# Performance work log

Hardware: AMD Instinct MI355X
Metric: run time of the kernel (lower is better)

The kernel has to match this reference:

```python
import jax, jax.numpy as jnp
import numpy as np

N = 100000
E = 1600000
B = 64
NUM_CLASSES = 10


def setup_inputs() -> dict:
    key = jax.random.key(0)
    ks = jax.random.split(key, 8)
    x = jax.random.normal(ks[0], (N, 5), dtype=jnp.float32)
    edge_index = jax.random.randint(ks[1], (2, E), 0, N, dtype=jnp.int64)
    batch = jnp.sort(jax.random.randint(ks[2], (N,), 0, B, dtype=jnp.int64))

    def glorot(k, fan_in, fan_out):
        s = jnp.sqrt(6.0 / (fan_in + fan_out)).astype(jnp.float32)
        return jax.random.uniform(k, (fan_in, fan_out), jnp.float32, -s, s)

    dims = [(5, 32), (32, 64), (64, 128), (128, 256)]
    Ws = [glorot(jax.random.fold_in(ks[3], i), a, b) for i, (a, b) in enumerate(dims)]
    bs = [jnp.zeros((b,), jnp.float32) for (_, b) in dims]
    fc1_w = glorot(ks[4], 256, 100)
    fc1_b = jnp.zeros((100,), jnp.float32)
    fc2_w = glorot(ks[5], 100, NUM_CLASSES)
    fc2_b = jnp.zeros((NUM_CLASSES,), jnp.float32)
    return {
        'x': x, 'edge_index': edge_index, 'batch': batch,
        'W1': Ws[0], 'b1': bs[0], 'W2': Ws[1], 'b2': bs[1],
        'W3': Ws[2], 'b3': bs[2], 'W4': Ws[3], 'b4': bs[3],
        'fc1_w': fc1_w, 'fc1_b': fc1_b, 'fc2_w': fc2_w, 'fc2_b': fc2_b,
    }


def _gcn_conv(x, W, b, src, dst, dinv):
    h = x @ W                                   # [N, out]
    norm = (dinv[src] * dinv[dst])[:, None]      # [E, 1]
    msg = h[src] * norm                          # gather + scale
    agg = jax.ops.segment_sum(msg, dst, num_segments=N)
    agg = agg + h * (dinv * dinv)[:, None]       # self-loop contribution
    return agg + b


def reference(x, edge_index, batch, W1, b1, W2, b2, W3, b3, W4, b4,
              fc1_w, fc1_b, fc2_w, fc2_b):
    src, dst = edge_index[0], edge_index[1]
    # degree including self-loop
    deg = jax.ops.segment_sum(jnp.ones((E,), jnp.float32), dst, num_segments=N) + 1.0
    dinv = jax.lax.rsqrt(deg)

    h = jax.nn.relu(_gcn_conv(x, W1, b1, src, dst, dinv))
    # mesh_unpool with pool target 0 -> identity
    h = jax.nn.relu(_gcn_conv(h, W2, b2, src, dst, dinv))
    h = jax.nn.relu(_gcn_conv(h, W3, b3, src, dst, dinv))
    h = jax.nn.relu(_gcn_conv(h, W4, b4, src, dst, dinv))

    # global mean pool over graphs
    sums = jax.ops.segment_sum(h, batch, num_segments=B)
    cnt = jax.ops.segment_sum(jnp.ones((N,), jnp.float32), batch, num_segments=B)
    pooled = sums / jnp.maximum(cnt, 1.0)[:, None]

    h = jax.nn.relu(pooled @ fc1_w + fc1_b)
    return jax.nn.log_softmax(h @ fc2_w + fc2_b, axis=-1)
```

## Files before the change

kernel.cpp:

```cpp
#include <hip/hip_runtime.h>
#include <hip/hip_bf16.h>
#include <cmath>

#define NN 100000
#define NE 1600000
#define NBATCH 64
#define NB 391
#define NBP 512
#define BCAP 5120
#define NPAD (NB * BCAP)

typedef __attribute__((ext_vector_type(8))) short bf16x8;
typedef __attribute__((ext_vector_type(4))) float f32x4;

__device__ __forceinline__ void atomAdd(float* p, float v) {
  unsafeAtomicAdd(p, v);
}

__device__ __forceinline__ unsigned short f2bf(float f) {
  __hip_bfloat16 h = __float2bfloat16(f);
  union { __hip_bfloat16 h; unsigned short u; } cv; cv.h = h; return cv.u;
}
__device__ __forceinline__ float bflo(unsigned int u) { return __uint_as_float(u << 16); }
__device__ __forceinline__ float bfhi(unsigned int u) { return __uint_as_float(u & 0xffff0000u); }

__global__ __launch_bounds__(256) void k_bin(const int* __restrict__ src,
    const int* __restrict__ dst, int* __restrict__ bucketCnt, uint2* __restrict__ pairs,
    const float* __restrict__ W2, const float* __restrict__ W3, const float* __restrict__ W4,
    unsigned short* __restrict__ Wt2, unsigned short* __restrict__ Wt3,
    unsigned short* __restrict__ Wt4) {
  __shared__ int hist[NBP];
  __shared__ int scn[NBP];
  __shared__ int ofs[NBP];
  __shared__ int gbase[NBP];
  __shared__ uint2 buf[4096];
  const int base = blockIdx.x * 4096;
  const int n = (NE - base < 4096) ? NE - base : 4096;
  for (int i = threadIdx.x; i < NBP; i += 256) hist[i] = 0;
  __syncthreads();

  int myS[16], myD[16];
  int nloc = 0;
  for (int i = threadIdx.x, j = 0; i < n; i += 256, ++j) {
    myS[j] = src[base + i];
    myD[j] = dst[base + i];
    atomicAdd(&hist[myD[j] >> 8], 1);
    nloc = j + 1;
  }
  __syncthreads();

  scn[threadIdx.x] = hist[threadIdx.x];
  scn[threadIdx.x + 256] = hist[threadIdx.x + 256];
  __syncthreads();
  for (int off = 1; off < NBP; off <<= 1) {
    const int i0 = threadIdx.x, i1 = threadIdx.x + 256;
    int t0 = (i0 >= off) ? scn[i0 - off] : 0;
    int t1 = (i1 >= off) ? scn[i1 - off] : 0;
    __syncthreads();
    scn[i0] += t0;
    scn[i1] += t1;
    __syncthreads();
  }
  ofs[threadIdx.x] = scn[threadIdx.x] - hist[threadIdx.x];
  ofs[threadIdx.x + 256] = scn[threadIdx.x + 256] - hist[threadIdx.x + 256];
  for (int b = threadIdx.x; b < NB; b += 256) {
    int c = hist[b];
    if (c) gbase[b] = b * BCAP + atomicAdd(&bucketCnt[b], c);
  }
  __syncthreads();

  for (int j = 0; j < nloc; ++j) {
    int b = myD[j] >> 8;
    int slot = atomicAdd(&ofs[b], 1);
    buf[slot] = make_uint2((unsigned)myS[j], (unsigned)myD[j]);
  }
  __syncthreads();

  for (int i = threadIdx.x; i < n; i += 256) {
    uint2 p = buf[i];
    int b = (int)(p.y >> 8);
    int ex = scn[b] - hist[b];
    pairs[gbase[b] + (i - ex)] = p;
  }

  int idx = blockIdx.x * 256 + threadIdx.x;
  if (idx < 2048) {
    int k = idx / 64, m = idx - k * 64;
    Wt2[m * 32 + k] = f2bf(W2[idx]);
  } else if (idx < 10240) {
    int j = idx - 2048;
    int k = j / 128, m = j - k * 128;
    Wt3[m * 64 + k] = f2bf(W3[j]);
  } else if (idx < 43008) {
    int j = idx - 10240;
    int k = j / 256, m = j - k * 256;
    Wt4[m * 128 + k] = f2bf(W4[j]);
  }
}

__global__ __launch_bounds__(256) void k_cntfill(const uint2* __restrict__ pairs,
    const int* __restrict__ bucketCnt, const int* __restrict__ batch,
    const float* __restrict__ x, int* __restrict__ rowbeg, int* __restrict__ rowend,
    float* __restrict__ dinv, int* __restrict__ csrc, float* __restrict__ pcnt,
    unsigned short* __restrict__ xs8) {
  __shared__ int c[256];
  __shared__ int scn[256];
  __shared__ int rowb[256];
  __shared__ int ofs[256];
  __shared__ int h[64];
  const int tid = threadIdx.x;
  c[tid] = 0; ofs[tid] = 0;
  if (tid < 64) h[tid] = 0;
  __syncthreads();
  const int b = blockIdx.x;
  const int s = b * BCAP;
  const int e = s + bucketCnt[b];
  for (int i = s + tid; i < e; i += 256) atomicAdd(&c[pairs[i].y & 255], 1);
  __syncthreads();
  const int v = c[tid];
  scn[tid] = v;
  __syncthreads();
  for (int off = 1; off < 256; off <<= 1) {
    int t = (tid >= off) ? scn[tid - off] : 0;
    __syncthreads();
    scn[tid] += t;
    __syncthreads();
  }
  rowb[tid] = s + scn[tid] - v;
  const int node = b * 256 + tid;
  rowbeg[node] = rowb[tid];
  rowend[node] = rowb[tid] + v;
  if (node < NN) {
    const float di = rsqrtf((float)v + 1.0f);
    dinv[node] = di;
    float f0 = x[(size_t)node * 5 + 0] * di;
    float f1 = x[(size_t)node * 5 + 1] * di;
    float f2 = x[(size_t)node * 5 + 2] * di;
    float f3 = x[(size_t)node * 5 + 3] * di;
    float f4 = x[(size_t)node * 5 + 4] * di;
    uint4 o;
    o.x = (unsigned int)f2bf(f0) | ((unsigned int)f2bf(f1) << 16);
    o.y = (unsigned int)f2bf(f2) | ((unsigned int)f2bf(f3) << 16);
    o.z = (unsigned int)f2bf(f4);
    o.w = 0u;
    *(uint4*)(xs8 + (size_t)node * 8) = o;
    atomicAdd(&h[batch[node]], 1);
  }
  __syncthreads();
  for (int i = s + tid; i < e; i += 256) {
    uint2 p = pairs[i];
    int t = (int)(p.y & 255);
    int pos = rowb[t] + atomicAdd(&ofs[t], 1);
    csrc[pos] = (int)p.x;
  }
  if (tid < 64 && h[tid]) atomAdd(&pcnt[tid], (float)h[tid]);
}

__global__ __launch_bounds__(256) void k_l1v(const unsigned short* __restrict__ xs8,
    const int* __restrict__ rowbeg, const int* __restrict__ rowend,
    const int* __restrict__ csrc, const float* __restrict__ dinv,
    const float* __restrict__ W, const float* __restrict__ b,
    unsigned short* __restrict__ outp) {
  __shared__ float w_s[160];
  __shared__ float b_s[32];
  const int tid = threadIdx.x;
  if (tid < 160) w_s[tid] = W[tid];
  if (tid < 32) b_s[tid] = b[tid];
  __syncthreads();
  const int r = blockIdx.x * 256 + tid;
  if (r >= NN) return;
  const float di = dinv[r];
  float a0, a1, a2, a3, a4, c0 = 0.f, c1 = 0.f, c2 = 0.f, c3 = 0.f, c4 = 0.f;
  {
    const uint4 v = *(const uint4*)(xs8 + (size_t)r * 8);
    a0 = bflo(v.x); a1 = bfhi(v.x); a2 = bflo(v.y); a3 = bfhi(v.y); a4 = bflo(v.z);
  }
  int e = rowbeg[r];
  const int e1 = rowend[r];
  for (; e + 2 <= e1; e += 2) {
    const int s0 = csrc[e], s1 = csrc[e + 1];
    const uint4 u0 = *(const uint4*)(xs8 + (size_t)s0 * 8);
    const uint4 u1 = *(const uint4*)(xs8 + (size_t)s1 * 8);
    a0 += bflo(u0.x); a1 += bfhi(u0.x); a2 += bflo(u0.y); a3 += bfhi(u0.y); a4 += bflo(u0.z);
    c0 += bflo(u1.x); c1 += bfhi(u1.x); c2 += bflo(u1.y); c3 += bfhi(u1.y); c4 += bflo(u1.z);
  }
  if (e < e1) {
    const int s0 = csrc[e];
    const uint4 u0 = *(const uint4*)(xs8 + (size_t)s0 * 8);
    a0 += bflo(u0.x); a1 += bfhi(u0.x); a2 += bflo(u0.y); a3 += bfhi(u0.y); a4 += bflo(u0.z);
  }
  const float f0 = (a0 + c0) * di, f1 = (a1 + c1) * di, f2 = (a2 + c2) * di,
              f3 = (a3 + c3) * di, f4 = (a4 + c4) * di;
  unsigned int o[16];
#pragma unroll
  for (int j = 0; j < 16; ++j) {
    const int cA = 2 * j, cB = 2 * j + 1;
    float sA = b_s[cA] + f0 * w_s[cA]       + f1 * w_s[32 + cA]  + f2 * w_s[64 + cA]
                       + f3 * w_s[96 + cA]  + f4 * w_s[128 + cA];
    float sB = b_s[cB] + f0 * w_s[cB]       + f1 * w_s[32 + cB]  + f2 * w_s[64 + cB]
                       + f3 * w_s[96 + cB]  + f4 * w_s[128 + cB];
    sA = fmaxf(sA, 0.f) * di; sB = fmaxf(sB, 0.f) * di;
    o[j] = (unsigned int)f2bf(sA) | ((unsigned int)f2bf(sB) << 16);
  }
  uint4* op = (uint4*)(outp + (size_t)r * 32);
  op[0] = *(uint4*)&o[0];
  op[1] = *(uint4*)&o[4];
  op[2] = *(uint4*)&o[8];
  op[3] = *(uint4*)&o[12];
}

template<int K>
__global__ __launch_bounds__(256) void k_gatherb(const unsigned short* __restrict__ in,
    const int* __restrict__ rowbeg, const int* __restrict__ rowend,
    const int* __restrict__ csrc, const float* __restrict__ dinv,
    unsigned short* __restrict__ agg) {
  constexpr int TPR = K / 8;
  constexpr int RPB = 256 / TPR;
  const int r = blockIdx.x * RPB + threadIdx.x / TPR;
  if (r >= NN) return;
  const int c = (threadIdx.x % TPR) * 8;
  const float di = dinv[r];
  float a0[8], a1[8];
  {
    const uint4 v = *(const uint4*)(in + (size_t)r * K + c);
    a0[0] = bflo(v.x); a0[1] = bfhi(v.x);
    a0[2] = bflo(v.y); a0[3] = bfhi(v.y);
    a0[4] = bflo(v.z); a0[5] = bfhi(v.z);
    a0[6] = bflo(v.w); a0[7] = bfhi(v.w);
#pragma unroll
    for (int j = 0; j < 8; ++j) a1[j] = 0.f;
  }
  int e = rowbeg[r];
  const int e1 = rowend[r];
  for (; e + 4 <= e1; e += 4) {
    const int s0 = csrc[e], s1 = csrc[e + 1], s2 = csrc[e + 2], s3 = csrc[e + 3];
    const uint4 v0 = *(const uint4*)(in + (size_t)s0 * K + c);
    const uint4 v1 = *(const uint4*)(in + (size_t)s1 * K + c);
    const uint4 v2 = *(const uint4*)(in + (size_t)s2 * K + c);
    const uint4 v3 = *(const uint4*)(in + (size_t)s3 * K + c);
    a0[0] += bflo(v0.x); a0[1] += bfhi(v0.x); a0[2] += bflo(v0.y); a0[3] += bfhi(v0.y);
    a0[4] += bflo(v0.z); a0[5] += bfhi(v0.z); a0[6] += bflo(v0.w); a0[7] += bfhi(v0.w);
    a1[0] += bflo(v1.x); a1[1] += bfhi(v1.x); a1[2] += bflo(v1.y); a1[3] += bfhi(v1.y);
    a1[4] += bflo(v1.z); a1[5] += bfhi(v1.z); a1[6] += bflo(v1.w); a1[7] += bfhi(v1.w);
    a0[0] += bflo(v2.x); a0[1] += bfhi(v2.x); a0[2] += bflo(v2.y); a0[3] += bfhi(v2.y);
    a0[4] += bflo(v2.z); a0[5] += bfhi(v2.z); a0[6] += bflo(v2.w); a0[7] += bfhi(v2.w);
    a1[0] += bflo(v3.x); a1[1] += bfhi(v3.x); a1[2] += bflo(v3.y); a1[3] += bfhi(v3.y);
    a1[4] += bflo(v3.z); a1[5] += bfhi(v3.z); a1[6] += bflo(v3.w); a1[7] += bfhi(v3.w);
  }
  for (; e < e1; ++e) {
    const int s0 = csrc[e];
    const uint4 v0 = *(const uint4*)(in + (size_t)s0 * K + c);
    a0[0] += bflo(v0.x); a0[1] += bfhi(v0.x); a0[2] += bflo(v0.y); a0[3] += bfhi(v0.y);
    a0[4] += bflo(v0.z); a0[5] += bfhi(v0.z); a0[6] += bflo(v0.w); a0[7] += bfhi(v0.w);
  }
  uint4 o;
  o.x = (unsigned int)f2bf((a0[0] + a1[0]) * di) | ((unsigned int)f2bf((a0[1] + a1[1]) * di) << 16);
  o.y = (unsigned int)f2bf((a0[2] + a1[2]) * di) | ((unsigned int)f2bf((a0[3] + a1[3]) * di) << 16);
  o.z = (unsigned int)f2bf((a0[4] + a1[4]) * di) | ((unsigned int)f2bf((a0[5] + a1[5]) * di) << 16);
  o.w = (unsigned int)f2bf((a0[6] + a1[6]) * di) | ((unsigned int)f2bf((a0[7] + a1[7]) * di) << 16);
  *(uint4*)(agg + (size_t)r * K + c) = o;
}

template<int K, int M, int MODE>
__global__ __launch_bounds__(256) void k_gemm_mfma(const unsigned short* __restrict__ agg,
    const unsigned short* __restrict__ Wt, const float* __restrict__ bias,
    const float* __restrict__ dinv, unsigned short* __restrict__ outp,
    const int* __restrict__ batch, float* __restrict__ pooled) {
  constexpr int KP = K + 8;
  constexpr int KC = 32;
  constexpr int WP = KC + 8;
  constexpr int CTW = M / 64;
  constexpr int C8 = K / 8;
  __shared__ unsigned short a_s[64 * KP];
  __shared__ unsigned short w_s[M * WP];
  const int r0 = blockIdx.x * 64;
  const int tid = threadIdx.x;

  for (int idx = tid; idx < 64 * C8; idx += 256) {
    int row = idx / C8, cc = (idx % C8) * 8;
    uint4 v = {0u, 0u, 0u, 0u};
    if (r0 + row < NN) v = *(const uint4*)(agg + (size_t)(r0 + row) * K + cc);
    *(uint4*)&a_s[row * KP + cc] = v;
  }

  const int wave = tid >> 6, lane = tid & 63;
  const int m16 = lane & 15, q = lane >> 4;
  f32x4 acc[4][CTW];
#pragma unroll
  for (int rt = 0; rt < 4; ++rt)
#pragma unroll
    for (int ct = 0; ct < CTW; ++ct) acc[rt][ct] = (f32x4){0.f, 0.f, 0.f, 0.f};

  for (int kc = 0; kc < K; kc += KC) {
    __syncthreads();
    for (int idx = tid; idx < M * (KC / 8); idx += 256) {
      int m = idx / (KC / 8), cc = (idx % (KC / 8)) * 8;
      uint4 v = *(const uint4*)(Wt + (size_t)m * K + kc + cc);
      *(uint4*)&w_s[m * WP + cc] = v;
    }
    __syncthreads();
    bf16x8 bfr[CTW];
#pragma unroll
    for (int ct = 0; ct < CTW; ++ct)
      bfr[ct] = *(const bf16x8*)&w_s[(wave * (M / 4) + ct * 16 + m16) * WP + q * 8];
#pragma unroll
    for (int rt = 0; rt < 4; ++rt) {
      bf16x8 afr = *(const bf16x8*)&a_s[(rt * 16 + m16) * KP + kc + q * 8];
#pragma unroll
      for (int ct = 0; ct < CTW; ++ct)
        acc[rt][ct] = __builtin_amdgcn_mfma_f32_16x16x32_bf16(afr, bfr[ct], acc[rt][ct], 0, 0, 0);
    }
  }

  if constexpr (MODE == 1) {
    const int rlast = (r0 + 63 < NN) ? r0 + 63 : NN - 1;
    const int bmin = batch[r0];
    const int bmax = batch[rlast];
    int rowb[4][4];
#pragma unroll
    for (int rt = 0; rt < 4; ++rt)
#pragma unroll
      for (int reg = 0; reg < 4; ++reg) {
        const int row = r0 + rt * 16 + q * 4 + reg;
        rowb[rt][reg] = (row < NN) ? batch[row] : -1;
      }
#pragma unroll
    for (int ct = 0; ct < CTW; ++ct) {
      const int col = wave * (M / 4) + ct * 16 + m16;
      const float bv = bias[col];
      for (int b = bmin; b <= bmax; ++b) {
        float s = 0.f;
#pragma unroll
        for (int rt = 0; rt < 4; ++rt)
#pragma unroll
          for (int reg = 0; reg < 4; ++reg)
            if (rowb[rt][reg] == b) s += fmaxf(acc[rt][ct][reg] + bv, 0.f);
        s += __shfl_xor(s, 16);
        s += __shfl_xor(s, 32);
        if (q == 0) atomAdd(&pooled[b * M + col], s);
      }
    }
  } else {
    float dsc[4][4];
#pragma unroll
    for (int rt = 0; rt < 4; ++rt)
#pragma unroll
      for (int reg = 0; reg < 4; ++reg) {
        const int row = r0 + rt * 16 + q * 4 + reg;
        dsc[rt][reg] = (row < NN) ? dinv[row] : 0.f;
      }
#pragma unroll
    for (int rt = 0; rt < 4; ++rt) {
#pragma unroll
      for (int ct = 0; ct < CTW; ++ct) {
        const int col = wave * (M / 4) + ct * 16 + m16;
        const float bv = bias[col];
#pragma unroll
        for (int reg = 0; reg < 4; ++reg) {
          const int row = r0 + rt * 16 + q * 4 + reg;
          if (row < NN) {
            float vv = fmaxf(acc[rt][ct][reg] + bv, 0.f) * dsc[rt][reg];
            outp[(size_t)row * M + col] = f2bf(vv);
          }
        }
      }
    }
  }
}

__global__ __launch_bounds__(128) void k_mlp(const float* __restrict__ pooled,
    const float* __restrict__ cnt, const float* __restrict__ w1,
    const float* __restrict__ b1, const float* __restrict__ w2,
    const float* __restrict__ b2, float* __restrict__ out) {
  __shared__ float p[256];
  __shared__ float h1[100];
  __shared__ float lo[10];
  const int b = blockIdx.x;
  const float inv = 1.0f / fmaxf(cnt[b], 1.0f);
  for (int i = threadIdx.x; i < 256; i += 128) p[i] = pooled[b * 256 + i] * inv;
  __syncthreads();
  for (int j = threadIdx.x; j < 100; j += 128) {
    float s = b1[j];
    for (int k = 0; k < 256; ++k) s += p[k] * w1[k * 100 + j];
    h1[j] = fmaxf(s, 0.f);
  }
  __syncthreads();
  if (threadIdx.x < 10) {
    int j = threadIdx.x;
    float s = b2[j];
    for (int k = 0; k < 100; ++k) s += h1[k] * w2[k * 10 + j];
    lo[j] = s;
  }
  __syncthreads();
  if (threadIdx.x == 0) {
    float m = lo[0];
    for (int j = 1; j < 10; ++j) m = fmaxf(m, lo[j]);
    float ssum = 0.f;
    for (int j = 0; j < 10; ++j) ssum += expf(lo[j] - m);
    float lse = m + logf(ssum);
    for (int j = 0; j < 10; ++j) out[b * 10 + j] = lo[j] - lse;
  }
}

extern "C" void kernel_launch(void* const* d_in, const int* in_sizes, int n_in,
                              void* d_out, int out_size, void* d_ws, size_t ws_size,
                              hipStream_t stream) {
  const float* x     = (const float*)d_in[0];
  const int*   ei    = (const int*)d_in[1];
  const int*   batch = (const int*)d_in[2];
  const float* W1 = (const float*)d_in[3];  const float* b1 = (const float*)d_in[4];
  const float* W2 = (const float*)d_in[5];  const float* b2 = (const float*)d_in[6];
  const float* W3 = (const float*)d_in[7];  const float* b3 = (const float*)d_in[8];
  const float* W4 = (const float*)d_in[9];  const float* b4 = (const float*)d_in[10];
  const float* fc1w = (const float*)d_in[11]; const float* fc1b = (const float*)d_in[12];
  const float* fc2w = (const float*)d_in[13]; const float* fc2b = (const float*)d_in[14];
  float* out = (float*)d_out;

  const int* src = ei;
  const int* dst = ei + NE;

  float* ws = (float*)d_ws;
  float* pooled = ws;
  float* pcnt   = pooled + 16384;
  int*   bucketCnt = (int*)(pcnt + 64);
  float* dinv   = (float*)(bucketCnt + 512);
  int*   rowbeg = (int*)(dinv + 100352);
  int*   rowend = rowbeg + 100352;
  int*   csrc   = rowend + 100352;
  uint2* pairs  = (uint2*)(csrc + NPAD);
  unsigned short* xs8 = (unsigned short*)(pairs + NPAD);
  unsigned short* F0  = xs8 + 800768;
  unsigned short* F1  = F0 + (size_t)NN * 32;
  unsigned short* F2  = F1 + (size_t)NN * 64;
  unsigned short* AG  = F2 + (size_t)NN * 128;
  unsigned short* Wt2 = AG + (size_t)NN * 128;
  unsigned short* Wt3 = Wt2 + 32 * 64;
  unsigned short* Wt4 = Wt3 + 64 * 128;

  (void)hipMemsetAsync(pooled, 0, (16384 + 64 + 512) * sizeof(float), stream);
  k_bin<<<(NE + 4095) / 4096, 256, 0, stream>>>(src, dst, bucketCnt, pairs,
                                                W2, W3, W4, Wt2, Wt3, Wt4);
  k_cntfill<<<NB, 256, 0, stream>>>(pairs, bucketCnt, batch, x,
                                    rowbeg, rowend, dinv, csrc, pcnt, xs8);

  k_l1v<<<(NN + 255) / 256, 256, 0, stream>>>(xs8, rowbeg, rowend, csrc, dinv, W1, b1, F0);

  k_gatherb<32><<<(NN + 63) / 64, 256, 0, stream>>>(F0, rowbeg, rowend, csrc, dinv, AG);
  k_gemm_mfma<32, 64, 0><<<(NN + 63) / 64, 256, 0, stream>>>(
      AG, Wt2, b2, dinv, F1, nullptr, nullptr);

  k_gatherb<64><<<(NN + 31) / 32, 256, 0, stream>>>(F1, rowbeg, rowend, csrc, dinv, AG);
  k_gemm_mfma<64, 128, 0><<<(NN + 63) / 64, 256, 0, stream>>>(
      AG, Wt3, b3, dinv, F2, nullptr, nullptr);

  k_gatherb<128><<<(NN + 15) / 16, 256, 0, stream>>>(F2, rowbeg, rowend, csrc, dinv, AG);
  k_gemm_mfma<128, 256, 1><<<(NN + 63) / 64, 256, 0, stream>>>(
      AG, Wt4, b4, dinv, nullptr, batch, pooled);

  k_mlp<<<NBATCH, 128, 0, stream>>>(pooled, pcnt, fc1w, fc1b, fc2w, fc2b, out);
}
```

Baseline: 321.5 us.

## Switch bf16 storage to fp16 with packed half-precision gather accumulation

Replaces bf16 storage of features and weights with fp16 throughout. The neighbor gathers now accumulate directly in packed f16x8 vectors instead of unpacking to fp32, and the GEMM uses the f16 MFMA instruction. The gather loop is also unrolled to 8 neighbors with 4 accumulators. This cuts the ALU cost of unpack, convert and repack in the memory-bound gathers, at the cost of fp16 range limits and reduced accumulation precision for high-degree nodes.

```diff
diff --git a/kernel.cpp b/kernel.cpp
--- a/kernel.cpp
+++ b/kernel.cpp
@@ -10,25 +10,17 @@
 #define BCAP 5120
 #define NPAD (NB * BCAP)
 
-typedef __attribute__((ext_vector_type(8))) short bf16x8;
+typedef __attribute__((ext_vector_type(8))) _Float16 f16x8;
 typedef __attribute__((ext_vector_type(4))) float f32x4;
 
 __device__ __forceinline__ void atomAdd(float* p, float v) {
   unsafeAtomicAdd(p, v);
 }
-
-__device__ __forceinline__ unsigned short f2bf(float f) {
-  __hip_bfloat16 h = __float2bfloat16(f);
-  union { __hip_bfloat16 h; unsigned short u; } cv; cv.h = h; return cv.u;
-}
-__device__ __forceinline__ float bflo(unsigned int u) { return __uint_as_float(u << 16); }
-__device__ __forceinline__ float bfhi(unsigned int u) { return __uint_as_float(u & 0xffff0000u); }
 
 __global__ __launch_bounds__(256) void k_bin(const int* __restrict__ src,
     const int* __restrict__ dst, int* __restrict__ bucketCnt, uint2* __restrict__ pairs,
     const float* __restrict__ W2, const float* __restrict__ W3, const float* __restrict__ W4,
-    unsigned short* __restrict__ Wt2, unsigned short* __restrict__ Wt3,
-    unsigned short* __restrict__ Wt4) {
+    _Float16* __restrict__ Wt2, _Float16* __restrict__ Wt3, _Float16* __restrict__ Wt4) {
   __shared__ int hist[NBP];
   __shared__ int scn[NBP];
   __shared__ int ofs[NBP];
@@ -86,15 +78,15 @@
   int idx = blockIdx.x * 256 + threadIdx.x;
   if (idx < 2048) {
     int k = idx / 64, m = idx - k * 64;
-    Wt2[m * 32 + k] = f2bf(W2[idx]);
+    Wt2[m * 32 + k] = (_Float16)W2[idx];
   } else if (idx < 10240) {
     int j = idx - 2048;
     int k = j / 128, m = j - k * 128;
-    Wt3[m * 64 + k] = f2bf(W3[j]);
+    Wt3[m * 64 + k] = (_Float16)W3[j];
   } else if (idx < 43008) {
     int j = idx - 10240;
     int k = j / 256, m = j - k * 256;
-    Wt4[m * 128 + k] = f2bf(W4[j]);
+    Wt4[m * 128 + k] = (_Float16)W4[j];
   }
 }
 
@@ -102,7 +94,7 @@
     const int* __restrict__ bucketCnt, const int* __restrict__ batch,
     const float* __restrict__ x, int* __restrict__ rowbeg, int* __restrict__ rowend,
     float* __restrict__ dinv, int* __restrict__ csrc, float* __restrict__ pcnt,
-    unsigned short* __restrict__ xs8) {
+    _Float16* __restrict__ xs8) {
   __shared__ int c[256];
   __shared__ int scn[256];
   __shared__ int rowb[256];
@@ -133,17 +125,13 @@
   if (node < NN) {
     const float di = rsqrtf((float)v + 1.0f);
     dinv[node] = di;
-    float f0 = x[(size_t)node * 5 + 0] * di;
-    float f1 = x[(size_t)node * 5 + 1] * di;
-    float f2 = x[(size_t)node * 5 + 2] * di;
-    float f3 = x[(size_t)node * 5 + 3] * di;
-    float f4 = x[(size_t)node * 5 + 4] * di;
-    uint4 o;
-    o.x = (unsigned int)f2bf(f0) | ((unsigned int)f2bf(f1) << 16);
-    o.y = (unsigned int)f2bf(f2) | ((unsigned int)f2bf(f3) << 16);
-    o.z = (unsigned int)f2bf(f4);
-    o.w = 0u;
-    *(uint4*)(xs8 + (size_t)node * 8) = o;
+    f16x8 o = {0, 0, 0, 0, 0, 0, 0, 0};
+    o[0] = (_Float16)(x[(size_t)node * 5 + 0] * di);
+    o[1] = (_Float16)(x[(size_t)node * 5 + 1] * di);
+    o[2] = (_Float16)(x[(size_t)node * 5 + 2] * di);
+    o[3] = (_Float16)(x[(size_t)node * 5 + 3] * di);
+    o[4] = (_Float16)(x[(size_t)node * 5 + 4] * di);
+    *(f16x8*)(xs8 + (size_t)node * 8) = o;
     atomicAdd(&h[batch[node]], 1);
   }
   __syncthreads();
@@ -156,11 +144,11 @@
   if (tid < 64 && h[tid]) atomAdd(&pcnt[tid], (float)h[tid]);
 }
 
-__global__ __launch_bounds__(256) void k_l1v(const unsigned short* __restrict__ xs8,
+__global__ __launch_bounds__(256) void k_l1v(const _Float16* __restrict__ xs8,
     const int* __restrict__ rowbeg, const int* __restrict__ rowend,
     const int* __restrict__ csrc, const float* __restrict__ dinv,
     const float* __restrict__ W, const float* __restrict__ b,
-    unsigned short* __restrict__ outp) {
+    _Float16* __restrict__ outp) {
   __shared__ float w_s[160];
   __shared__ float b_s[32];
   const int tid = threadIdx.x;
@@ -170,109 +158,89 @@
   const int r = blockIdx.x * 256 + tid;
   if (r >= NN) return;
   const float di = dinv[r];
-  float a0, a1, a2, a3, a4, c0 = 0.f, c1 = 0.f, c2 = 0.f, c3 = 0.f, c4 = 0.f;
-  {
-    const uint4 v = *(const uint4*)(xs8 + (size_t)r * 8);
-    a0 = bflo(v.x); a1 = bfhi(v.x); a2 = bflo(v.y); a3 = bfhi(v.y); a4 = bflo(v.z);
-  }
+  f16x8 a = *(const f16x8*)(xs8 + (size_t)r * 8);
+  f16x8 cacc = {0, 0, 0, 0, 0, 0, 0, 0};
   int e = rowbeg[r];
   const int e1 = rowend[r];
   for (; e + 2 <= e1; e += 2) {
     const int s0 = csrc[e], s1 = csrc[e + 1];
-    const uint4 u0 = *(const uint4*)(xs8 + (size_t)s0 * 8);
-    const uint4 u1 = *(const uint4*)(xs8 + (size_t)s1 * 8);
-    a0 += bflo(u0.x); a1 += bfhi(u0.x); a2 += bflo(u0.y); a3 += bfhi(u0.y); a4 += bflo(u0.z);
-    c0 += bflo(u1.x); c1 += bfhi(u1.x); c2 += bflo(u1.y); c3 += bfhi(u1.y); c4 += bflo(u1.z);
-  }
-  if (e < e1) {
-    const int s0 = csrc[e];
-    const uint4 u0 = *(const uint4*)(xs8 + (size_t)s0 * 8);
-    a0 += bflo(u0.x); a1 += bfhi(u0.x); a2 += bflo(u0.y); a3 += bfhi(u0.y); a4 += bflo(u0.z);
-  }
-  const float f0 = (a0 + c0) * di, f1 = (a1 + c1) * di, f2 = (a2 + c2) * di,
-              f3 = (a3 + c3) * di, f4 = (a4 + c4) * di;
-  unsigned int o[16];
-#pragma unroll
-  for (int j = 0; j < 16; ++j) {
-    const int cA = 2 * j, cB = 2 * j + 1;
-    float sA = b_s[cA] + f0 * w_s[cA]       + f1 * w_s[32 + cA]  + f2 * w_s[64 + cA]
-                       + f3 * w_s[96 + cA]  + f4 * w_s[128 + cA];
-    float sB = b_s[cB] + f0 * w_s[cB]       + f1 * w_s[32 + cB]  + f2 * w_s[64 + cB]
-                       + f3 * w_s[96 + cB]  + f4 * w_s[128 + cB];
-    sA = fmaxf(sA, 0.f) * di; sB = fmaxf(sB, 0.f) * di;
-    o[j] = (unsigned int)f2bf(sA) | ((unsigned int)f2bf(sB) << 16);
+    a    += *(const f16x8*)(xs8 + (size_t)s0 * 8);
+    cacc += *(const f16x8*)(xs8 + (size_t)s1 * 8);
+  }
+  if (e < e1) a += *(const f16x8*)(xs8 + (size_t)csrc[e] * 8);
+  a += cacc;
+  const float f0 = (float)a[0] * di, f1 = (float)a[1] * di, f2 = (float)a[2] * di,
+              f3 = (float)a[3] * di, f4 = (float)a[4] * di;
+  _Float16 ov[32];
+#pragma unroll
+  for (int j = 0; j < 32; ++j) {
+    float s = b_s[j] + f0 * w_s[j] + f1 * w_s[32 + j] + f2 * w_s[64 + j]
+                     + f3 * w_s[96 + j] + f4 * w_s[128 + j];
+    ov[j] = (_Float16)(fmaxf(s, 0.f) * di);
   }
   uint4* op = (uint4*)(outp + (size_t)r * 32);
-  op[0] = *(uint4*)&o[0];
-  op[1] = *(uint4*)&o[4];
-  op[2] = *(uint4*)&o[8];
-  op[3] = *(uint4*)&o[12];
+  op[0] = *(uint4*)&ov[0];
+  op[1] = *(uint4*)&ov[8];
+  op[2] = *(uint4*)&ov[16];
+  op[3] = *(uint4*)&ov[24];
 }
 
 template<int K>
-__global__ __launch_bounds__(256) void k_gatherb(const unsigned short* __restrict__ in,
+__global__ __launch_bounds__(256) void k_gatherb(const _Float16* __restrict__ in,
     const int* __restrict__ rowbeg, const int* __restrict__ rowend,
     const int* __restrict__ csrc, const float* __restrict__ dinv,
-    unsigned short* __restrict__ agg) {
+    _Float16* __restrict__ agg) {
   constexpr int TPR = K / 8;
   constexpr int RPB = 256 / TPR;
   const int r = blockIdx.x * RPB + threadIdx.x / TPR;
   if (r >= NN) return;
   const int c = (threadIdx.x % TPR) * 8;
   const float di = dinv[r];
-  float a0[8], a1[8];
-  {
-    const uint4 v = *(const uint4*)(in + (size_t)r * K + c);
-    a0[0] = bflo(v.x); a0[1] = bfhi(v.x);
-    a0[2] = bflo(v.y); a0[3] = bfhi(v.y);
-    a0[4] = bflo(v.z); a0[5] = bfhi(v.z);
-    a0[6] = bflo(v.w); a0[7] = bfhi(v.w);
-#pragma unroll
-    for (int j = 0; j < 8; ++j) a1[j] = 0.f;
-  }
+  f16x8 a0 = *(const f16x8*)(in + (size_t)r * K + c);
+  f16x8 a1 = {0, 0, 0, 0, 0, 0, 0, 0};
+  f16x8 a2 = {0, 0, 0, 0, 0, 0, 0, 0};
+  f16x8 a3 = {0, 0, 0, 0, 0, 0, 0, 0};
   int e = rowbeg[r];
   const int e1 = rowend[r];
-  for (; e + 4 <= e1; e += 4) {
-    const int s0 = csrc[e], s1 = csrc[e + 1], s2 = csrc[e + 2], s3 = csrc[e + 3];
-    const uint4 v0 = *(const uint4*)(in + (size_t)s0 * K + c);
-    const uint4 v1 = *(const uint4*)(in + (size_t)s1 * K + c);
-    const uint4 v2 = *(const uint4*)(in + (size_t)s2 * K + c);
-    const uint4 v3 = *(const uint4*)(in + (size_t)s3 * K + c);
-    a0[0] += bflo(v0.x); a0[1] += bfhi(v0.x); a0[2] += bflo(v0.y); a0[3] += bfhi(v0.y);
-    a0[4] += bflo(v0.z); a0[5] += bfhi(v0.z); a0[6] += bflo(v0.w); a0[7] += bfhi(v0.w);
-    a1[0] += bflo(v1.x); a1[1] += bfhi(v1.x); a1[2] += bflo(v1.y); a1[3] += bfhi(v1.y);
-    a1[4] += bflo(v1.z); a1[5] += bfhi(v1.z); a1[6] += bflo(v1.w); a1[7] += bfhi(v1.w);
-    a0[0] += bflo(v2.x); a0[1] += bfhi(v2.x); a0[2] += bflo(v2.y); a0[3] += bfhi(v2.y);
-    a0[4] += bflo(v2.z); a0[5] += bfhi(v2.z); a0[6] += bflo(v2.w); a0[7] += bfhi(v2.w);
-    a1[0] += bflo(v3.x); a1[1] += bfhi(v3.x); a1[2] += bflo(v3.y); a1[3] += bfhi(v3.y);
-    a1[4] += bflo(v3.z); a1[5] += bfhi(v3.z); a1[6] += bflo(v3.w); a1[7] += bfhi(v3.w);
-  }
-  for (; e < e1; ++e) {
-    const int s0 = csrc[e];
-    const uint4 v0 = *(const uint4*)(in + (size_t)s0 * K + c);
-    a0[0] += bflo(v0.x); a0[1] += bfhi(v0.x); a0[2] += bflo(v0.y); a0[3] += bfhi(v0.y);
-    a0[4] += bflo(v0.z); a0[5] += bfhi(v0.z); a0[6] += bflo(v0.w); a0[7] += bfhi(v0.w);
-  }
-  uint4 o;
-  o.x = (unsigned int)f2bf((a0[0] + a1[0]) * di) | ((unsigned int)f2bf((a0[1] + a1[1]) * di) << 16);
-  o.y = (unsigned int)f2bf((a0[2] + a1[2]) * di) | ((unsigned int)f2bf((a0[3] + a1[3]) * di) << 16);
-  o.z = (unsigned int)f2bf((a0[4] + a1[4]) * di) | ((unsigned int)f2bf((a0[5] + a1[5]) * di) << 16);
-  o.w = (unsigned int)f2bf((a0[6] + a1[6]) * di) | ((unsigned int)f2bf((a0[7] + a1[7]) * di) << 16);
-  *(uint4*)(agg + (size_t)r * K + c) = o;
+  for (; e + 8 <= e1; e += 8) {
+    const int s0 = csrc[e],     s1 = csrc[e + 1], s2 = csrc[e + 2], s3 = csrc[e + 3];
+    const int s4 = csrc[e + 4], s5 = csrc[e + 5], s6 = csrc[e + 6], s7 = csrc[e + 7];
+    const f16x8 v0 = *(const f16x8*)(in + (size_t)s0 * K + c);
+    const f16x8 v1 = *(const f16x8*)(in + (size_t)s1 * K + c);
+    const f16x8 v2 = *(const f16x8*)(in + (size_t)s2 * K + c);
+    const f16x8 v3 = *(const f16x8*)(in + (size_t)s3 * K + c);
+    const f16x8 v4 = *(const f16x8*)(in + (size_t)s4 * K + c);
+    const f16x8 v5 = *(const f16x8*)(in + (size_t)s5 * K + c);
+    const f16x8 v6 = *(const f16x8*)(in + (size_t)s6 * K + c);
+    const f16x8 v7 = *(const f16x8*)(in + (size_t)s7 * K + c);
+    a0 += v0; a1 += v1; a2 += v2; a3 += v3;
+    a0 += v4; a1 += v5; a2 += v6; a3 += v7;
+  }
+  for (; e + 2 <= e1; e += 2) {
+    const int s0 = csrc[e], s1 = csrc[e + 1];
+    a0 += *(const f16x8*)(in + (size_t)s0 * K + c);
+    a1 += *(const f16x8*)(in + (size_t)s1 * K + c);
+  }
+  if (e < e1) a0 += *(const f16x8*)(in + (size_t)csrc[e] * K + c);
+  a0 = (a0 + a1) + (a2 + a3);
+  const _Float16 dh = (_Float16)di;
+  const f16x8 ds = {dh, dh, dh, dh, dh, dh, dh, dh};
+  a0 *= ds;
+  *(f16x8*)(agg + (size_t)r * K + c) = a0;
 }
 
 template<int K, int M, int MODE>
-__global__ __launch_bounds__(256) void k_gemm_mfma(const unsigned short* __restrict__ agg,
-    const unsigned short* __restrict__ Wt, const float* __restrict__ bias,
-    const float* __restrict__ dinv, unsigned short* __restrict__ outp,
+__global__ __launch_bounds__(256) void k_gemm_mfma(const _Float16* __restrict__ agg,
+    const _Float16* __restrict__ Wt, const float* __restrict__ bias,
+    const float* __restrict__ dinv, _Float16* __restrict__ outp,
     const int* __restrict__ batch, float* __restrict__ pooled) {
   constexpr int KP = K + 8;
   constexpr int KC = 32;
   constexpr int WP = KC + 8;
   constexpr int CTW = M / 64;
   constexpr int C8 = K / 8;
-  __shared__ unsigned short a_s[64 * KP];
-  __shared__ unsigned short w_s[M * WP];
+  __shared__ _Float16 a_s[64 * KP];
+  __shared__ _Float16 w_s[M * WP];
   const int r0 = blockIdx.x * 64;
   const int tid = threadIdx.x;
 
@@ -299,16 +267,16 @@
       *(uint4*)&w_s[m * WP + cc] = v;
     }
     __syncthreads();
-    bf16x8 bfr[CTW];
+    f16x8 bfr[CTW];
 #pragma unroll
     for (int ct = 0; ct < CTW; ++ct)
-      bfr[ct] = *(const bf16x8*)&w_s[(wave * (M / 4) + ct * 16 + m16) * WP + q * 8];
+      bfr[ct] = *(const f16x8*)&w_s[(wave * (M / 4) + ct * 16 + m16) * WP + q * 8];
 #pragma unroll
     for (int rt = 0; rt < 4; ++rt) {
-      bf16x8 afr = *(const bf16x8*)&a_s[(rt * 16 + m16) * KP + kc + q * 8];
+      f16x8 afr = *(const f16x8*)&a_s[(rt * 16 + m16) * KP + kc + q * 8];
 #pragma unroll
       for (int ct = 0; ct < CTW; ++ct)
-        acc[rt][ct] = __builtin_amdgcn_mfma_f32_16x16x32_bf16(afr, bfr[ct], acc[rt][ct], 0, 0, 0);
+        acc[rt][ct] = __builtin_amdgcn_mfma_f32_16x16x32_f16(afr, bfr[ct], acc[rt][ct], 0, 0, 0);
     }
   }
 
@@ -360,7 +328,7 @@
           const int row = r0 + rt * 16 + q * 4 + reg;
           if (row < NN) {
             float vv = fmaxf(acc[rt][ct][reg] + bv, 0.f) * dsc[rt][reg];
-            outp[(size_t)row * M + col] = f2bf(vv);
+            outp[(size_t)row * M + col] = (_Float16)vv;
           }
         }
       }
@@ -428,14 +396,14 @@
   int*   rowend = rowbeg + 100352;
   int*   csrc   = rowend + 100352;
   uint2* pairs  = (uint2*)(csrc + NPAD);
-  unsigned short* xs8 = (unsigned short*)(pairs + NPAD);
-  unsigned short* F0  = xs8 + 800768;
-  unsigned short* F1  = F0 + (size_t)NN * 32;
-  unsigned short* F2  = F1 + (size_t)NN * 64;
-  unsigned short* AG  = F2 + (size_t)NN * 128;
-  unsigned short* Wt2 = AG + (size_t)NN * 128;
-  unsigned short* Wt3 = Wt2 + 32 * 64;
-  unsigned short* Wt4 = Wt3 + 64 * 128;
+  _Float16* xs8 = (_Float16*)(pairs + NPAD);
+  _Float16* F0  = xs8 + 800768;
+  _Float16* F1  = F0 + (size_t)NN * 32;
+  _Float16* F2  = F1 + (size_t)NN * 64;
+  _Float16* AG  = F2 + (size_t)NN * 128;
+  _Float16* Wt2 = AG + (size_t)NN * 128;
+  _Float16* Wt3 = Wt2 + 32 * 64;
+  _Float16* Wt4 = Wt3 + 64 * 128;
 
   (void)hipMemsetAsync(pooled, 0, (16384 + 64 + 512) * sizeof(float), stream);
   k_bin<<<(NE + 4095) / 4096, 256, 0, stream>>>(src, dst, bucketCnt, pairs,
```

Result: no change. 318.7 us (-0.9%).
